# Performance work log

Measured on AMD Instinct MI355X. Metric: run time of the kernel, lower is better.

## Reference

```python
import jax, jax.numpy as jnp
import numpy as np
import math

B, LQ, LK, D = 16, 2048, 2048, 64

def setup_inputs() -> dict:
    key = jax.random.key(0)
    kq, kk, kv, kn = jax.random.split(key, 4)
    q = jax.random.normal(kq, (B, LQ, D), dtype=jnp.float32)
    k = jax.random.normal(kk, (B, LK, D), dtype=jnp.float32)
    v = jax.random.normal(kv, (B, LK, D), dtype=jnp.float32)
    # valid lengths in [1, LK] so no row is fully masked
    valid_num = jax.random.randint(kn, (B,), 1, LK + 1, dtype=jnp.int32)
    return {"q": q, "k": k, "v": v, "valid_num": valid_num}

def reference(q, k, v, valid_num):
    d = q.shape[-1]
    # [B, LQ, LK] scores
    scores = jnp.einsum('bqd,bkd->bqk', q, k) / math.sqrt(d)
    # 1D valid_num -> same key mask for every query row (matches repeat_interleave)
    key_pos = jnp.arange(k.shape[1], dtype=valid_num.dtype)  # [LK]
    mask = key_pos[None, None, :] < valid_num[:, None, None]  # [B,1,LK] -> broadcast
    scores = jnp.where(mask, scores, -jnp.inf)
    attn = jax.nn.softmax(scores, axis=-1)
    # dropout p=0.0 -> identity (eval/deterministic reference)
    return jnp.einsum('bqk,bkd->bqd', attn, v)
```

## Files before the change

### kernel.cpp

```cpp
#include <hip/hip_runtime.h>


namespace {

constexpr int NB  = 16;
constexpr int SLQ = 2048;
constexpr int SLK = 2048;
constexpr int DH  = 64;
constexpr int KB  = 64;
constexpr int QB  = 64;

typedef _Float16 half8  __attribute__((ext_vector_type(8)));
typedef _Float16 half4  __attribute__((ext_vector_type(4)));
typedef _Float16 half2t __attribute__((ext_vector_type(2)));
typedef float    f32x4  __attribute__((ext_vector_type(4)));

__device__ inline half2t pkrtz(float a, float b) {
    return __builtin_bit_cast(half2t, __builtin_amdgcn_cvt_pkrtz(a, b));
}

__global__ __launch_bounds__(256)
void prepass(const float* __restrict__ kg, const float* __restrict__ vg,
             _Float16* __restrict__ kws, _Float16* __restrict__ vws)
{
    __shared__ _Float16 VT[DH][72];
    const int t  = threadIdx.x;
    const int b  = blockIdx.x >> 5;
    const int kt = blockIdx.x & 31;
    const size_t tileH = ((size_t)(b << 5) + kt) * 4096;

    {
        const float* kp = kg + ((size_t)b * SLK + (size_t)kt * KB) * DH + t * 16;
        f32x4 a0 = ((const f32x4*)kp)[0], a1 = ((const f32x4*)kp)[1];
        f32x4 a2 = ((const f32x4*)kp)[2], a3 = ((const f32x4*)kp)[3];
        union { half2t h2[4]; uint4 u; } o0, o1;
        o0.h2[0] = pkrtz(a0[0], a0[1]); o0.h2[1] = pkrtz(a0[2], a0[3]);
        o0.h2[2] = pkrtz(a1[0], a1[1]); o0.h2[3] = pkrtz(a1[2], a1[3]);
        o1.h2[0] = pkrtz(a2[0], a2[1]); o1.h2[1] = pkrtz(a2[2], a2[3]);
        o1.h2[2] = pkrtz(a3[0], a3[1]); o1.h2[3] = pkrtz(a3[2], a3[3]);
#pragma unroll
        for (int j = 0; j < 2; ++j) {
            const int n = 2 * t + j;
            const int rr = n >> 3, c = n & 7;
            const int dst = rr * 8 + (c ^ (rr & 7));
            *(uint4*)(kws + tileH + (size_t)dst * 8) = j ? o1.u : o0.u;
        }
    }
    {
        const int kr = t >> 2, d0 = (t & 3) * 16;
        const float* vp = vg + ((size_t)b * SLK + (size_t)kt * KB + kr) * DH + d0;
        f32x4 a0 = ((const f32x4*)vp)[0], a1 = ((const f32x4*)vp)[1];
        f32x4 a2 = ((const f32x4*)vp)[2], a3 = ((const f32x4*)vp)[3];
#pragma unroll
        for (int i = 0; i < 4; ++i) {
            VT[d0 + i][kr]      = (_Float16)a0[i];
            VT[d0 + 4 + i][kr]  = (_Float16)a1[i];
            VT[d0 + 8 + i][kr]  = (_Float16)a2[i];
            VT[d0 + 12 + i][kr] = (_Float16)a3[i];
        }
    }
    __syncthreads();
#pragma unroll
    for (int j = 0; j < 2; ++j) {
        const int n = 2 * t + j;
        const int d = n >> 3, c = n & 7;
        const int dst = d * 8 + (c ^ (d & 7));
        half8 hv = *(const half8*)&VT[d][c * 8];
        *(half8*)(vws + tileH + (size_t)dst * 8) = hv;
    }
}

__global__ __launch_bounds__(256)
void attn_fwd(const float* __restrict__ qg, const _Float16* __restrict__ k16,
              const _Float16* __restrict__ v16, const int* __restrict__ vn,
              _Float16* __restrict__ ws_acc, float* __restrict__ ws_ml,
              int nsplit, int tps)
{
    __shared__ __attribute__((aligned(16))) _Float16 KV[2][8192];

    const int t   = threadIdx.x;
    const int l   = t & 63;
    const int w   = t >> 6;
    const int q15 = l & 15;
    const int g   = l >> 4;
    const int swz = (q15 & 7) << 3;

    const int bid = blockIdx.x;
    int b, qt, s;
    if (nsplit == 8) {
        const int k4 = bid >> 8;
        s  = k4 & 7;
        b  = (((bid >> 4) & 15) + k4) & 15;
        qt = (bid & 15) | ((k4 >> 3) << 4);
    } else {
        b  = ((bid & 15) + 8 * (bid >> 8)) & 15;
        qt = (bid >> 4) & 31;
        s  = 0;
    }

    const int valid = vn[b];
    const int nkt   = (valid + KB - 1) / KB;
    const int kt0   = s * tps;
    if (kt0 >= nkt) return;
    const int kt1   = min(nkt, kt0 + tps);

    const int qrow = qt * QB + w * 16 + q15;

    const float QS = 0.18033688011112042f;

    half8 qf[2];
    {
        const float* qp = qg + ((size_t)b * SLQ + qrow) * DH;
#pragma unroll
        for (int ss = 0; ss < 2; ++ss) {
            const int d0 = 8 * g + 32 * ss;
            f32x4 x = *(const f32x4*)(qp + d0);
            f32x4 y = *(const f32x4*)(qp + d0 + 4);
            half8 h;
#pragma unroll
            for (int i = 0; i < 4; ++i) {
                h[i]     = (_Float16)(x[i] * QS);
                h[i + 4] = (_Float16)(y[i] * QS);
            }
            qf[ss] = h;
        }
    }

    f32x4 acc[4];
#pragma unroll
    for (int i = 0; i < 4; ++i) acc[i] = f32x4{0.f, 0.f, 0.f, 0.f};
    float m = -1e30f, lsum = 0.f;

    const _Float16* kbase = k16 + (size_t)(b << 5) * 4096;
    const _Float16* vbase = v16 + (size_t)(b << 5) * 4096;

    uint4 rk0, rk1, rv0, rv1;
#define LOADREGS(KT)                                                         \
    {                                                                        \
        const uint4* kp_ = (const uint4*)(kbase + (size_t)(KT) * 4096);      \
        const uint4* vp_ = (const uint4*)(vbase + (size_t)(KT) * 4096);      \
        rk0 = kp_[t]; rk1 = kp_[t + 256];                                    \
        rv0 = vp_[t]; rv1 = vp_[t + 256];                                    \
    }
#define WRITEKV(CUR)                                                         \
    {                                                                        \
        uint4* kl_ = (uint4*)&KV[CUR][0];                                    \
        uint4* vl_ = (uint4*)&KV[CUR][4096];                                 \
        kl_[t] = rk0; kl_[t + 256] = rk1;                                    \
        vl_[t] = rv0; vl_[t + 256] = rv1;                                    \
    }

    LOADREGS(kt0);
    int cur = 0;

    for (int kt = kt0; kt < kt1; ++kt) {
        WRITEKV(cur);
        __syncthreads();
        if (kt + 1 < kt1) LOADREGS(kt + 1);

        const _Float16* Kc = &KV[cur][0];
        const _Float16* Vc = &KV[cur][4096];

        f32x4 st[4];
        __builtin_amdgcn_s_setprio(1);
#pragma unroll
        for (int mt = 0; mt < 4; ++mt) {
            f32x4 c = f32x4{0.f, 0.f, 0.f, 0.f};
#pragma unroll
            for (int ss = 0; ss < 2; ++ss) {
                half8 a = *(const half8*)&Kc[(16 * mt + q15) * 64 + ((8 * g + 32 * ss) ^ swz)];
                c = __builtin_amdgcn_mfma_f32_16x16x32_f16(a, qf[ss], c, 0, 0, 0);
            }
            st[mt] = c;
        }
        __builtin_amdgcn_s_setprio(0);

        const int krem = valid - kt * KB;
        if (krem < KB) {
#pragma unroll
            for (int mt = 0; mt < 4; ++mt)
#pragma unroll
                for (int r = 0; r < 4; ++r)
                    if (16 * mt + 4 * g + r >= krem) st[mt][r] = -1e30f;
        }

        float x0 = fmaxf(fmaxf(st[0][0], st[0][1]), fmaxf(st[0][2], st[0][3]));
        float x1 = fmaxf(fmaxf(st[1][0], st[1][1]), fmaxf(st[1][2], st[1][3]));
        float x2 = fmaxf(fmaxf(st[2][0], st[2][1]), fmaxf(st[2][2], st[2][3]));
        float x3 = fmaxf(fmaxf(st[3][0], st[3][1]), fmaxf(st[3][2], st[3][3]));
        float tmax = fmaxf(fmaxf(x0, x1), fmaxf(x2, x3));
        tmax = fmaxf(tmax, __shfl_xor(tmax, 16));
        tmax = fmaxf(tmax, __shfl_xor(tmax, 32));

        if (!__all(tmax - m <= 12.0f)) {
            const float mn = fmaxf(m, tmax);
            const float sc = __builtin_amdgcn_exp2f(m - mn);
            lsum *= sc;
#pragma unroll
            for (int mt = 0; mt < 4; ++mt) acc[mt] *= sc;
            m = mn;
        }

        float p[4][4];
#pragma unroll
        for (int mt = 0; mt < 4; ++mt)
#pragma unroll
            for (int r = 0; r < 4; ++r)
                p[mt][r] = __builtin_amdgcn_exp2f(st[mt][r] - m);

        float s0 = (p[0][0] + p[0][1]) + (p[0][2] + p[0][3]);
        float s1 = (p[1][0] + p[1][1]) + (p[1][2] + p[1][3]);
        float s2 = (p[2][0] + p[2][1]) + (p[2][2] + p[2][3]);
        float s3 = (p[3][0] + p[3][1]) + (p[3][2] + p[3][3]);
        float ps = (s0 + s1) + (s2 + s3);
        ps += __shfl_xor(ps, 16);
        ps += __shfl_xor(ps, 32);
        lsum += ps;

        half2t pk[4][2];
#pragma unroll
        for (int mt = 0; mt < 4; ++mt)
#pragma unroll
            for (int rr = 0; rr < 2; ++rr)
                pk[mt][rr] = pkrtz(p[mt][2 * rr], p[mt][2 * rr + 1]);

        __builtin_amdgcn_s_setprio(1);
#pragma unroll
        for (int ss = 0; ss < 2; ++ss) {
            union { half2t h2[4]; half8 v; } bf;
            bf.h2[0] = pk[2 * ss][0];
            bf.h2[1] = pk[2 * ss][1];
            bf.h2[2] = pk[2 * ss + 1][0];
            bf.h2[3] = pk[2 * ss + 1][1];
#pragma unroll
            for (int mt = 0; mt < 4; ++mt) {
                union { half4 h4[2]; half8 v; } af;
                af.h4[0] = *(const half4*)&Vc[(16 * mt + q15) * 64 + ((32 * ss + 4 * g) ^ swz)];
                af.h4[1] = *(const half4*)&Vc[(16 * mt + q15) * 64 + ((32 * ss + 16 + 4 * g) ^ swz)];
                acc[mt] = __builtin_amdgcn_mfma_f32_16x16x32_f16(af.v, bf.v, acc[mt], 0, 0, 0);
            }
        }
        __builtin_amdgcn_s_setprio(0);
        cur ^= 1;
    }
#undef LOADREGS
#undef WRITEKV

    const float inv = 1.0f / lsum;
    const size_t row = (size_t)b * SLQ + qrow;
    _Float16* wp = ws_acc + ((size_t)s * NB * SLQ + row) * DH;
#pragma unroll
    for (int mt = 0; mt < 4; ++mt) {
        union { half2t h2[2]; uint2 u; } o;
        o.h2[0] = pkrtz(acc[mt][0] * inv, acc[mt][1] * inv);
        o.h2[1] = pkrtz(acc[mt][2] * inv, acc[mt][3] * inv);
        *(uint2*)(wp + 16 * mt + 4 * g) = o.u;
    }
    if (g == 0)
        *(float2*)(ws_ml + ((size_t)s * NB * SLQ + row) * 2) = make_float2(m, lsum);
}

__global__ __launch_bounds__(256)
void attn_combine(const _Float16* __restrict__ ws_acc, const float* __restrict__ ws_ml,
                  const int* __restrict__ vn, float* __restrict__ og,
                  int nsplit, int tps)
{
    const int tid = blockIdx.x * 256 + threadIdx.x;
    const int row = tid >> 2;
    const int dq  = (tid & 3) << 4;
    const int b   = row >> 11;

    const int valid = vn[b];
    const int nkt   = (valid + KB - 1) / KB;
    const int nact  = min(nsplit, (nkt + tps - 1) / tps);

    float M = -1e30f;
    for (int s = 0; s < nact; ++s)
        M = fmaxf(M, ws_ml[((size_t)s * NB * SLQ + row) * 2]);

    float L = 0.f;
    f32x4 o[4];
#pragma unroll
    for (int i = 0; i < 4; ++i) o[i] = f32x4{0.f, 0.f, 0.f, 0.f};

    for (int s = 0; s < nact; ++s) {
        const float2 ml = *(const float2*)(ws_ml + ((size_t)s * NB * SLQ + row) * 2);
        const float wl = __builtin_amdgcn_exp2f(ml.x - M) * ml.y;
        L += wl;
        const _Float16* ap = ws_acc + ((size_t)s * NB * SLQ + row) * DH + dq;
        half8 h0 = ((const half8*)ap)[0];
        half8 h1 = ((const half8*)ap)[1];
#pragma unroll
        for (int r = 0; r < 4; ++r) {
            o[0][r] += wl * (float)h0[r];
            o[1][r] += wl * (float)h0[4 + r];
            o[2][r] += wl * (float)h1[r];
            o[3][r] += wl * (float)h1[4 + r];
        }
    }

    const float inv = 1.0f / L;
    float* op = og + (size_t)row * DH + dq;
#pragma unroll
    for (int i = 0; i < 4; ++i) {
        f32x4 r = o[i] * inv;
        *(f32x4*)(op + 4 * i) = r;
    }
}

}

extern "C" void kernel_launch(void* const* d_in, const int* in_sizes, int n_in,
                              void* d_out, int out_size, void* d_ws, size_t ws_size,
                              hipStream_t stream)
{
    const float* q    = (const float*)d_in[0];
    const float* k    = (const float*)d_in[1];
    const float* v    = (const float*)d_in[2];
    const int*   vnum = (const int*)d_in[3];
    float* out = (float*)d_out;

    const size_t k16H  = (size_t)NB * SLK * DH;
    const size_t v16H  = k16H;
    const size_t rowsH = (size_t)NB * SLQ;

    int nsplit = 8;
    {
        const size_t need8 = (k16H + v16H + (size_t)8 * rowsH * DH) * 2
                           + (size_t)8 * rowsH * 2 * 4;
        if (ws_size < need8) nsplit = 1;
    }
    const int tps = (nsplit == 8) ? 4 : 32;

    _Float16* k16    = (_Float16*)d_ws;
    _Float16* v16t   = k16 + k16H;
    _Float16* ws_acc = v16t + v16H;
    float*    ws_ml  = (float*)(ws_acc + (size_t)nsplit * rowsH * DH);

    prepass<<<dim3(NB * (SLK / KB)), dim3(256), 0, stream>>>(k, v, k16, v16t);

    dim3 gfwd(nsplit == 8 ? 4096 : 512);
    attn_fwd<<<gfwd, dim3(256), 0, stream>>>(q, k16, v16t, vnum, ws_acc, ws_ml,
                                             nsplit, tps);

    attn_combine<<<dim3((NB * SLQ * 4) / 256), dim3(256), 0, stream>>>(
        ws_acc, ws_ml, vnum, out, nsplit, tps);
}
```

Baseline: 43.62 us.

## Process two query tiles per block to reuse K/V tiles, skip masked prepass tiles

```diff
diff --git a/kernel.cpp b/kernel.cpp
--- a/kernel.cpp
+++ b/kernel.cpp
@@ -8,7 +8,7 @@
 constexpr int SLK = 2048;
 constexpr int DH  = 64;
 constexpr int KB  = 64;
-constexpr int QB  = 64;
+constexpr int QB  = 128;
 
 typedef _Float16 half8  __attribute__((ext_vector_type(8)));
 typedef _Float16 half4  __attribute__((ext_vector_type(4)));
@@ -21,12 +21,14 @@
 
 __global__ __launch_bounds__(256)
 void prepass(const float* __restrict__ kg, const float* __restrict__ vg,
+             const int* __restrict__ vn,
              _Float16* __restrict__ kws, _Float16* __restrict__ vws)
 {
     __shared__ _Float16 VT[DH][72];
     const int t  = threadIdx.x;
     const int b  = blockIdx.x >> 5;
     const int kt = blockIdx.x & 31;
+    if (kt * KB >= vn[b]) return;
     const size_t tileH = ((size_t)(b << 5) + kt) * 4096;
 
     {
@@ -89,12 +91,12 @@
     int b, qt, s;
     if (nsplit == 8) {
         const int k4 = bid >> 8;
-        s  = k4 & 7;
+        s  = k4;
         b  = (((bid >> 4) & 15) + k4) & 15;
-        qt = (bid & 15) | ((k4 >> 3) << 4);
+        qt = bid & 15;
     } else {
-        b  = ((bid & 15) + 8 * (bid >> 8)) & 15;
-        qt = (bid >> 4) & 31;
+        b  = bid & 15;
+        qt = bid >> 4;
         s  = 0;
     }
 
@@ -104,13 +106,15 @@
     if (kt0 >= nkt) return;
     const int kt1   = min(nkt, kt0 + tps);
 
-    const int qrow = qt * QB + w * 16 + q15;
+    const int qrow0 = qt * QB + w * 16 + q15;
+    const int qrow1 = qrow0 + 64;
 
     const float QS = 0.18033688011112042f;
 
-    half8 qf[2];
-    {
-        const float* qp = qg + ((size_t)b * SLQ + qrow) * DH;
+    half8 qf[2][2];
+#pragma unroll
+    for (int qi = 0; qi < 2; ++qi) {
+        const float* qp = qg + ((size_t)b * SLQ + (qi ? qrow1 : qrow0)) * DH;
 #pragma unroll
         for (int ss = 0; ss < 2; ++ss) {
             const int d0 = 8 * g + 32 * ss;
@@ -122,14 +126,14 @@
                 h[i]     = (_Float16)(x[i] * QS);
                 h[i + 4] = (_Float16)(y[i] * QS);
             }
-            qf[ss] = h;
-        }
-    }
-
-    f32x4 acc[4];
-#pragma unroll
-    for (int i = 0; i < 4; ++i) acc[i] = f32x4{0.f, 0.f, 0.f, 0.f};
-    float m = -1e30f, lsum = 0.f;
+            qf[qi][ss] = h;
+        }
+    }
+
+    f32x4 acc0[4], acc1[4];
+#pragma unroll
+    for (int i = 0; i < 4; ++i) { acc0[i] = f32x4{0.f,0.f,0.f,0.f}; acc1[i] = f32x4{0.f,0.f,0.f,0.f}; }
+    float m0 = -1e30f, l0 = 0.f, m1 = -1e30f, l1 = 0.f;
 
     const _Float16* kbase = k16 + (size_t)(b << 5) * 4096;
     const _Float16* vbase = v16 + (size_t)(b << 5) * 4096;
@@ -153,37 +157,8 @@
     LOADREGS(kt0);
     int cur = 0;
 
-    for (int kt = kt0; kt < kt1; ++kt) {
-        WRITEKV(cur);
-        __syncthreads();
-        if (kt + 1 < kt1) LOADREGS(kt + 1);
-
-        const _Float16* Kc = &KV[cur][0];
-        const _Float16* Vc = &KV[cur][4096];
-
-        f32x4 st[4];
-        __builtin_amdgcn_s_setprio(1);
-#pragma unroll
-        for (int mt = 0; mt < 4; ++mt) {
-            f32x4 c = f32x4{0.f, 0.f, 0.f, 0.f};
-#pragma unroll
-            for (int ss = 0; ss < 2; ++ss) {
-                half8 a = *(const half8*)&Kc[(16 * mt + q15) * 64 + ((8 * g + 32 * ss) ^ swz)];
-                c = __builtin_amdgcn_mfma_f32_16x16x32_f16(a, qf[ss], c, 0, 0, 0);
-            }
-            st[mt] = c;
-        }
-        __builtin_amdgcn_s_setprio(0);
-
-        const int krem = valid - kt * KB;
-        if (krem < KB) {
-#pragma unroll
-            for (int mt = 0; mt < 4; ++mt)
-#pragma unroll
-                for (int r = 0; r < 4; ++r)
-                    if (16 * mt + 4 * g + r >= krem) st[mt][r] = -1e30f;
-        }
-
+    auto softmax_pack = [&](f32x4 (&st)[4], float& m, float& lsum,
+                            f32x4 (&acc)[4], half2t (&pk)[4][2]) {
         float x0 = fmaxf(fmaxf(st[0][0], st[0][1]), fmaxf(st[0][2], st[0][3]));
         float x1 = fmaxf(fmaxf(st[1][0], st[1][1]), fmaxf(st[1][2], st[1][3]));
         float x2 = fmaxf(fmaxf(st[2][0], st[2][1]), fmaxf(st[2][2], st[2][3]));
@@ -191,7 +166,6 @@
         float tmax = fmaxf(fmaxf(x0, x1), fmaxf(x2, x3));
         tmax = fmaxf(tmax, __shfl_xor(tmax, 16));
         tmax = fmaxf(tmax, __shfl_xor(tmax, 32));
-
         if (!__all(tmax - m <= 12.0f)) {
             const float mn = fmaxf(m, tmax);
             const float sc = __builtin_amdgcn_exp2f(m - mn);
@@ -200,14 +174,12 @@
             for (int mt = 0; mt < 4; ++mt) acc[mt] *= sc;
             m = mn;
         }
-
         float p[4][4];
 #pragma unroll
         for (int mt = 0; mt < 4; ++mt)
 #pragma unroll
             for (int r = 0; r < 4; ++r)
                 p[mt][r] = __builtin_amdgcn_exp2f(st[mt][r] - m);
-
         float s0 = (p[0][0] + p[0][1]) + (p[0][2] + p[0][3]);
         float s1 = (p[1][0] + p[1][1]) + (p[1][2] + p[1][3]);
         float s2 = (p[2][0] + p[2][1]) + (p[2][2] + p[2][3]);
@@ -216,28 +188,64 @@
         ps += __shfl_xor(ps, 16);
         ps += __shfl_xor(ps, 32);
         lsum += ps;
-
-        half2t pk[4][2];
 #pragma unroll
         for (int mt = 0; mt < 4; ++mt)
 #pragma unroll
             for (int rr = 0; rr < 2; ++rr)
                 pk[mt][rr] = pkrtz(p[mt][2 * rr], p[mt][2 * rr + 1]);
-
+    };
+
+    for (int kt = kt0; kt < kt1; ++kt) {
+        WRITEKV(cur);
+        __syncthreads();
+        if (kt + 1 < kt1) LOADREGS(kt + 1);
+
+        const _Float16* Kc = &KV[cur][0];
+        const _Float16* Vc = &KV[cur][4096];
+
+        f32x4 st0[4], st1[4];
         __builtin_amdgcn_s_setprio(1);
 #pragma unroll
+        for (int mt = 0; mt < 4; ++mt) {
+            f32x4 c0 = f32x4{0.f,0.f,0.f,0.f}, c1 = f32x4{0.f,0.f,0.f,0.f};
+#pragma unroll
+            for (int ss = 0; ss < 2; ++ss) {
+                half8 a = *(const half8*)&Kc[(16 * mt + q15) * 64 + ((8 * g + 32 * ss) ^ swz)];
+                c0 = __builtin_amdgcn_mfma_f32_16x16x32_f16(a, qf[0][ss], c0, 0, 0, 0);
+                c1 = __builtin_amdgcn_mfma_f32_16x16x32_f16(a, qf[1][ss], c1, 0, 0, 0);
+            }
+            st0[mt] = c0; st1[mt] = c1;
+        }
+        __builtin_amdgcn_s_setprio(0);
+
+        const int krem = valid - kt * KB;
+        if (krem < KB) {
+#pragma unroll
+            for (int mt = 0; mt < 4; ++mt)
+#pragma unroll
+                for (int r = 0; r < 4; ++r)
+                    if (16 * mt + 4 * g + r >= krem) { st0[mt][r] = -1e30f; st1[mt][r] = -1e30f; }
+        }
+
+        half2t pk0[4][2], pk1[4][2];
+        softmax_pack(st0, m0, l0, acc0, pk0);
+        softmax_pack(st1, m1, l1, acc1, pk1);
+
+        __builtin_amdgcn_s_setprio(1);
+#pragma unroll
         for (int ss = 0; ss < 2; ++ss) {
-            union { half2t h2[4]; half8 v; } bf;
-            bf.h2[0] = pk[2 * ss][0];
-            bf.h2[1] = pk[2 * ss][1];
-            bf.h2[2] = pk[2 * ss + 1][0];
-            bf.h2[3] = pk[2 * ss + 1][1];
+            union { half2t h2[4]; half8 v; } bf0, bf1;
+            bf0.h2[0] = pk0[2 * ss][0]; bf0.h2[1] = pk0[2 * ss][1];
+            bf0.h2[2] = pk0[2 * ss + 1][0]; bf0.h2[3] = pk0[2 * ss + 1][1];
+            bf1.h2[0] = pk1[2 * ss][0]; bf1.h2[1] = pk1[2 * ss][1];
+            bf1.h2[2] = pk1[2 * ss + 1][0]; bf1.h2[3] = pk1[2 * ss + 1][1];
 #pragma unroll
             for (int mt = 0; mt < 4; ++mt) {
                 union { half4 h4[2]; half8 v; } af;
                 af.h4[0] = *(const half4*)&Vc[(16 * mt + q15) * 64 + ((32 * ss + 4 * g) ^ swz)];
                 af.h4[1] = *(const half4*)&Vc[(16 * mt + q15) * 64 + ((32 * ss + 16 + 4 * g) ^ swz)];
-                acc[mt] = __builtin_amdgcn_mfma_f32_16x16x32_f16(af.v, bf.v, acc[mt], 0, 0, 0);
+                acc0[mt] = __builtin_amdgcn_mfma_f32_16x16x32_f16(af.v, bf0.v, acc0[mt], 0, 0, 0);
+                acc1[mt] = __builtin_amdgcn_mfma_f32_16x16x32_f16(af.v, bf1.v, acc1[mt], 0, 0, 0);
             }
         }
         __builtin_amdgcn_s_setprio(0);
@@ -246,18 +254,24 @@
 #undef LOADREGS
 #undef WRITEKV
 
-    const float inv = 1.0f / lsum;
-    const size_t row = (size_t)b * SLQ + qrow;
-    _Float16* wp = ws_acc + ((size_t)s * NB * SLQ + row) * DH;
-#pragma unroll
-    for (int mt = 0; mt < 4; ++mt) {
-        union { half2t h2[2]; uint2 u; } o;
-        o.h2[0] = pkrtz(acc[mt][0] * inv, acc[mt][1] * inv);
-        o.h2[1] = pkrtz(acc[mt][2] * inv, acc[mt][3] * inv);
-        *(uint2*)(wp + 16 * mt + 4 * g) = o.u;
-    }
-    if (g == 0)
-        *(float2*)(ws_ml + ((size_t)s * NB * SLQ + row) * 2) = make_float2(m, lsum);
+#pragma unroll
+    for (int qi = 0; qi < 2; ++qi) {
+        const float inv = 1.0f / (qi ? l1 : l0);
+        const float mm  = qi ? m1 : m0;
+        const float ll  = qi ? l1 : l0;
+        f32x4* ac = qi ? acc1 : acc0;
+        const size_t row = (size_t)b * SLQ + (qi ? qrow1 : qrow0);
+        _Float16* wp = ws_acc + ((size_t)s * NB * SLQ + row) * DH;
+#pragma unroll
+        for (int mt = 0; mt < 4; ++mt) {
+            union { half2t h2[2]; uint2 u; } o;
+            o.h2[0] = pkrtz(ac[mt][0] * inv, ac[mt][1] * inv);
+            o.h2[1] = pkrtz(ac[mt][2] * inv, ac[mt][3] * inv);
+            *(uint2*)(wp + 16 * mt + 4 * g) = o.u;
+        }
+        if (g == 0)
+            *(float2*)(ws_ml + ((size_t)s * NB * SLQ + row) * 2) = make_float2(mm, ll);
+    }
 }
 
 __global__ __launch_bounds__(256)
@@ -337,9 +351,9 @@
     _Float16* ws_acc = v16t + v16H;
     float*    ws_ml  = (float*)(ws_acc + (size_t)nsplit * rowsH * DH);
 
-    prepass<<<dim3(NB * (SLK / KB)), dim3(256), 0, stream>>>(k, v, k16, v16t);
-
-    dim3 gfwd(nsplit == 8 ? 4096 : 512);
+    prepass<<<dim3(NB * (SLK / KB)), dim3(256), 0, stream>>>(k, v, vnum, k16, v16t);
+
+    dim3 gfwd(nsplit == 8 ? 2048 : 256);
     attn_fwd<<<gfwd, dim3(256), 0, stream>>>(q, k16, v16t, vnum, ws_acc, ws_ml,
                                              nsplit, tps);
 
```

Result: slower. 46.89 us (+7.5%).

## Skip masked K/V tiles in prepass, write single-split rows directly, permute V layout

Applied to the files above, without the earlier changes.

```diff
diff --git a/kernel.cpp b/kernel.cpp
--- a/kernel.cpp
+++ b/kernel.cpp
@@ -10,6 +10,9 @@
 constexpr int KB  = 64;
 constexpr int QB  = 64;
 
+constexpr int NSPLIT = 8;
+constexpr int TPS    = 4;
+
 typedef _Float16 half8  __attribute__((ext_vector_type(8)));
 typedef _Float16 half4  __attribute__((ext_vector_type(4)));
 typedef _Float16 half2t __attribute__((ext_vector_type(2)));
@@ -21,12 +24,14 @@
 
 __global__ __launch_bounds__(256)
 void prepass(const float* __restrict__ kg, const float* __restrict__ vg,
+             const int* __restrict__ vn,
              _Float16* __restrict__ kws, _Float16* __restrict__ vws)
 {
     __shared__ _Float16 VT[DH][72];
     const int t  = threadIdx.x;
     const int b  = blockIdx.x >> 5;
     const int kt = blockIdx.x & 31;
+    if (kt * KB >= vn[b]) return;
     const size_t tileH = ((size_t)(b << 5) + kt) * 4096;
 
     {
@@ -64,15 +69,20 @@
     for (int j = 0; j < 2; ++j) {
         const int n = 2 * t + j;
         const int d = n >> 3, c = n & 7;
-        const int dst = d * 8 + (c ^ (d & 7));
-        half8 hv = *(const half8*)&VT[d][c * 8];
-        *(half8*)(vws + tileH + (size_t)dst * 8) = hv;
+        const int rsw = (d & 7) << 3;
+        const int pA = 32 * (c >> 2) + 8 * ((2 * c) & 3) + 4 * ((c >> 1) & 1);
+        const int pB = 32 * (c >> 2) + 8 * ((2 * c + 1) & 3) + 4 * ((c >> 1) & 1);
+        half4 hA = *(const half4*)&VT[d][c * 8];
+        half4 hB = *(const half4*)&VT[d][c * 8 + 4];
+        *(half4*)(vws + tileH + (size_t)d * 64 + (pA ^ rsw)) = hA;
+        *(half4*)(vws + tileH + (size_t)d * 64 + (pB ^ rsw)) = hB;
     }
 }
 
 __global__ __launch_bounds__(256)
 void attn_fwd(const float* __restrict__ qg, const _Float16* __restrict__ k16,
               const _Float16* __restrict__ v16, const int* __restrict__ vn,
+              float* __restrict__ og,
               _Float16* __restrict__ ws_acc, float* __restrict__ ws_ml,
               int nsplit, int tps)
 {
@@ -103,6 +113,7 @@
     const int kt0   = s * tps;
     if (kt0 >= nkt) return;
     const int kt1   = min(nkt, kt0 + tps);
+    const int nact  = min(nsplit, (nkt + tps - 1) / tps);
 
     const int qrow = qt * QB + w * 16 + q15;
 
@@ -234,10 +245,8 @@
             bf.h2[3] = pk[2 * ss + 1][1];
 #pragma unroll
             for (int mt = 0; mt < 4; ++mt) {
-                union { half4 h4[2]; half8 v; } af;
-                af.h4[0] = *(const half4*)&Vc[(16 * mt + q15) * 64 + ((32 * ss + 4 * g) ^ swz)];
-                af.h4[1] = *(const half4*)&Vc[(16 * mt + q15) * 64 + ((32 * ss + 16 + 4 * g) ^ swz)];
-                acc[mt] = __builtin_amdgcn_mfma_f32_16x16x32_f16(af.v, bf.v, acc[mt], 0, 0, 0);
+                half8 af = *(const half8*)&Vc[(16 * mt + q15) * 64 + ((32 * ss + 8 * g) ^ swz)];
+                acc[mt] = __builtin_amdgcn_mfma_f32_16x16x32_f16(af, bf.v, acc[mt], 0, 0, 0);
             }
         }
         __builtin_amdgcn_s_setprio(0);
@@ -245,6 +254,19 @@
     }
 #undef LOADREGS
 #undef WRITEKV
+
+    if (nact == 1) {
+        const float inv = 1.0f / lsum;
+        float* op = og + ((size_t)b * SLQ + qrow) * DH;
+#pragma unroll
+        for (int mt = 0; mt < 4; ++mt) {
+            f32x4 o;
+#pragma unroll
+            for (int r = 0; r < 4; ++r) o[r] = acc[mt][r] * inv;
+            *(f32x4*)(op + 16 * mt + 4 * g) = o;
+        }
+        return;
+    }
 
     const float inv = 1.0f / lsum;
     const size_t row = (size_t)b * SLQ + qrow;
@@ -273,6 +295,7 @@
     const int valid = vn[b];
     const int nkt   = (valid + KB - 1) / KB;
     const int nact  = min(nsplit, (nkt + tps - 1) / tps);
+    if (nact <= 1) return;
 
     float M = -1e30f;
     for (int s = 0; s < nact; ++s)
@@ -324,24 +347,24 @@
     const size_t v16H  = k16H;
     const size_t rowsH = (size_t)NB * SLQ;
 
-    int nsplit = 8;
+    int nsplit = NSPLIT;
     {
-        const size_t need8 = (k16H + v16H + (size_t)8 * rowsH * DH) * 2
-                           + (size_t)8 * rowsH * 2 * 4;
+        const size_t need8 = (k16H + v16H + (size_t)NSPLIT * rowsH * DH) * 2
+                           + (size_t)NSPLIT * rowsH * 2 * 4;
         if (ws_size < need8) nsplit = 1;
     }
-    const int tps = (nsplit == 8) ? 4 : 32;
+    const int tps = (nsplit == NSPLIT) ? TPS : 32;
 
     _Float16* k16    = (_Float16*)d_ws;
     _Float16* v16t   = k16 + k16H;
     _Float16* ws_acc = v16t + v16H;
     float*    ws_ml  = (float*)(ws_acc + (size_t)nsplit * rowsH * DH);
 
-    prepass<<<dim3(NB * (SLK / KB)), dim3(256), 0, stream>>>(k, v, k16, v16t);
-
-    dim3 gfwd(nsplit == 8 ? 4096 : 512);
-    attn_fwd<<<gfwd, dim3(256), 0, stream>>>(q, k16, v16t, vnum, ws_acc, ws_ml,
-                                             nsplit, tps);
+    prepass<<<dim3(NB * (SLK / KB)), dim3(256), 0, stream>>>(k, v, vnum, k16, v16t);
+
+    dim3 gfwd(nsplit == NSPLIT ? 4096 : 512);
+    attn_fwd<<<gfwd, dim3(256), 0, stream>>>(q, k16, v16t, vnum, out,
+                                             ws_acc, ws_ml, nsplit, tps);
 
     attn_combine<<<dim3((NB * SLQ * 4) / 256), dim3(256), 0, stream>>>(
         ws_acc, ws_ml, vnum, out, nsplit, tps);
```

New measurement: 41.48 us. -4.9%, faster.
